# Optimization experiments

Measured on AMD Instinct MI355X. Metric: run time of the kernel, lower is better.

## Reference

```python
import jax, jax.numpy as jnp
import numpy as np

S, N, F, H, D, E, EL = 3, 100000, 64, 64, 64, 1000000, 500000
DP = 0.4


def setup_inputs() -> dict:
    key = jax.random.key(0)
    ks = jax.random.split(key, 12)
    inp = {
        'x': jax.random.normal(ks[0], (S, N, F), dtype=jnp.float32),
        'edge_index': jax.random.randint(ks[1], (S, 2, E), 0, N, dtype=jnp.int64 if jax.config.jax_enable_x64 else jnp.int32),
        'layer_edge_index': jax.random.randint(ks[2], (S - 1, 2, EL), 0, N, dtype=jnp.int64 if jax.config.jax_enable_x64 else jnp.int32),
        'deg_scalar': jax.random.uniform(ks[3], (S - 1,), minval=1.0, maxval=16.0, dtype=jnp.float32),
        'layer_W1': jax.random.normal(ks[4], (S, F, H), dtype=jnp.float32) * 0.05,
        'layer_b1': jnp.zeros((S, H), dtype=jnp.float32),
        'layer_W2': jax.random.normal(ks[5], (S, H, D), dtype=jnp.float32) * 0.05,
        'layer_b2': jnp.zeros((S, D), dtype=jnp.float32),
        'pred_W1': jax.random.normal(ks[6], (D, H), dtype=jnp.float32) * 0.05,
        'pred_b1': jnp.zeros((H,), dtype=jnp.float32),
        'pred_W2': jax.random.normal(ks[7], (H, 2), dtype=jnp.float32) * 0.05,
        'pred_b2': jnp.zeros((2,), dtype=jnp.float32),
    }
    return inp


def gcn_conv(h_in, src, dst, W, b, n):
    # standard GCNConv: D^-1/2 (A+I) D^-1/2 (X W) + b, messages flow src->dst
    h = h_in @ W  # [n, d_out]
    loop = jnp.arange(n, dtype=src.dtype)
    src2 = jnp.concatenate([src, loop])
    dst2 = jnp.concatenate([dst, loop])
    deg = jax.ops.segment_sum(jnp.ones_like(dst2, dtype=h.dtype), dst2, num_segments=n)
    dinv = jax.lax.rsqrt(jnp.maximum(deg, 1.0))  # self-loops guarantee deg>=1
    coef = (dinv[src2] * dinv[dst2])[:, None]
    out = jax.ops.segment_sum(h[src2] * coef, dst2, num_segments=n)
    return out + b


def gcn_net(x, ei, W1, b1, W2, b2, n):
    h = jax.nn.relu(gcn_conv(x, ei[0], ei[1], W1, b1, n))
    return gcn_conv(h, ei[0], ei[1], W2, b2, n)


def reference(x, edge_index, layer_edge_index, deg_scalar,
              layer_W1, layer_b1, layer_W2, layer_b2,
              pred_W1, pred_b1, pred_W2, pred_b2):
    last = None
    for i in range(S):
        lf = gcn_net(x[i], edge_index[i], layer_W1[i], layer_b1[i], layer_W2[i], layer_b2[i], N)  # [N, D]
        if i == 0:
            last = lf  # first surface: degrees empty -> no cross-layer aggregation
        else:
            recv, src = layer_edge_index[i - 1][0], layer_edge_index[i - 1][1]
            agg = lf + jax.ops.segment_sum(last[src], recv, num_segments=N)
            last = agg / deg_scalar[i - 1]  # faithful to source: scalar degrees[i]
    # F.dropout with default training=True -> active dropout; fixed key for determinism
    keep = jax.random.bernoulli(jax.random.key(42), 1.0 - DP, last.shape)
    x_emb = jnp.where(keep, last / (1.0 - DP), 0.0).astype(last.dtype)
    return gcn_net(x_emb, edge_index[-1], pred_W1, pred_b1, pred_W2, pred_b2, N)  # [N, 2]
```

## Files before the change

kernel.cpp:

```cpp
#include <hip/hip_runtime.h>
#include <hip/hip_fp16.h>

#define NN 100000
#define EE 1000000
#define ELL 500000
#define NF (NN*64)
#define NB_SCAN ((NN + 1023) / 1024)

#define OFF_CNT    100352
#define OFF_BSUM   200704
#define OFF_RPA    200832
#define OFF_COLA   301184
#define OFF_RPB    1301184
#define OFF_COLB   1401536
#define WS_SINGLE  (1301184 + 3*NF)
#define WS_DUAL    (2401536 + 4*NF)

__device__ __forceinline__ void threefry2x32(unsigned k0, unsigned k1, unsigned &x0, unsigned &x1){
  unsigned ks2 = k0 ^ k1 ^ 0x1BD11BDAu;
#define TF_R(R) { x0 += x1; x1 = (x1<<(R))|(x1>>(32-(R))); x1 ^= x0; }
  x0 += k0; x1 += k1;
  TF_R(13) TF_R(15) TF_R(26) TF_R(6)
  x0 += k1;  x1 += ks2 + 1u;
  TF_R(17) TF_R(29) TF_R(16) TF_R(24)
  x0 += ks2; x1 += k0 + 2u;
  TF_R(13) TF_R(15) TF_R(26) TF_R(6)
  x0 += k0;  x1 += k1 + 3u;
  TF_R(17) TF_R(29) TF_R(16) TF_R(24)
  x0 += k1;  x1 += ks2 + 4u;
  TF_R(13) TF_R(15) TF_R(26) TF_R(6)
  x0 += ks2; x1 += k0 + 5u;
#undef TF_R
}

__device__ __forceinline__ float dropout_val(float v, unsigned i){
  unsigned x0 = 0u, x1 = i;
  threefry2x32(0u, 42u, x0, x1);
  unsigned bits = x0 ^ x1;
  float u = __uint_as_float((bits >> 9) | 0x3f800000u) - 1.0f;
  return (u < 0.6f) ? v * (1.0f/0.6f) : 0.0f;
}

__global__ void k_probe(const int* __restrict__ ei, unsigned hostbits, float* __restrict__ out){
  if (threadIdx.x != 0 || blockIdx.x != 0) return;
  unsigned bits = hostbits;
  { unsigned a=0u, b=0u; threefry2x32(0u, 0u, a, b);
    if (a != 0x6b200159u || b != 0x99ba4efeu) bits |= 1u; }
  if (bits) out[0] = 1.0e4f * (float)bits;
}

__device__ __forceinline__ uint2 f4_to_h4(float4 v){
  __half2 lo = __floats2half2_rn(v.x, v.y);
  __half2 hi = __floats2half2_rn(v.z, v.w);
  uint2 r; r.x = *(unsigned*)&lo; r.y = *(unsigned*)&hi; return r;
}
__device__ __forceinline__ float4 h4_to_f4(uint2 u){
  __half2 lo = *(__half2*)&u.x;
  __half2 hi = *(__half2*)&u.y;
  float2 a = __half22float2(lo), b = __half22float2(hi);
  return make_float4(a.x, a.y, b.x, b.y);
}

__global__ void k_zero_int(int* __restrict__ p, int n){
  int i = blockIdx.x*256 + threadIdx.x;
  if (i < n) p[i] = 0;
}

__global__ void k_zerof(int* __restrict__ cnt, int n, int* __restrict__ flag){
  int i = blockIdx.x*256 + threadIdx.x;
  if (i < n) cnt[i] = 0;
  if (i == 0) *flag = 0;
}

__global__ void k_deg(const int* __restrict__ dst, int ne, int* __restrict__ cnt){
  int i = blockIdx.x*256 + threadIdx.x;
  if (i < ne) atomicAdd(&cnt[dst[i]], 1);
}

__global__ void k_degrank(const int* __restrict__ dst, int ne, int* __restrict__ cnt,
                          int* __restrict__ rank){
  int i = blockIdx.x*256 + threadIdx.x;
  if (i >= ne) return;
  rank[i] = atomicAdd(&cnt[dst[i]], 1);
}

__global__ void k_dinv(const int* __restrict__ cnt, float* __restrict__ dinv, int n){
  int i = blockIdx.x*256 + threadIdx.x;
  if (i < n) dinv[i] = 1.0f / sqrtf((float)(cnt[i] + 1));
}

__global__ __launch_bounds__(1024) void k_scanfused(const int* __restrict__ cnt, int* __restrict__ bsum,
                                                    int* __restrict__ flag, int* __restrict__ rowptr,
                                                    float* __restrict__ dinv, int computeDinv, int n){
  __shared__ int lds[1024];
  __shared__ int ps[128];
  int t = threadIdx.x;
  int i = blockIdx.x*1024 + t;
  int v = (i < n) ? cnt[i] : 0;
  if (computeDinv && i < n) dinv[i] = 1.0f / sqrtf((float)(v + 1));
  lds[t] = v;
  __syncthreads();
  for (int off = 1; off < 1024; off <<= 1){
    int x = (t >= off) ? lds[t - off] : 0;
    __syncthreads();
    lds[t] += x;
    __syncthreads();
  }
  int incl = lds[t];
  if (t == 1023){
    bsum[blockIdx.x] = lds[1023];
    __threadfence();
    atomicAdd(flag, 1);
  }
  if (t == 0){
    while (atomicAdd(flag, 0) < NB_SCAN) { }
  }
  __syncthreads();
  if (t < 128) ps[t] = (t < blockIdx.x) ? bsum[t] : 0;
  __syncthreads();
  if (t < 64) ps[t] += ps[t + 64];
  __syncthreads();
  if (t < 32) ps[t] += ps[t + 32];
  __syncthreads();
  if (t < 16) ps[t] += ps[t + 16];
  __syncthreads();
  if (t < 8)  ps[t] += ps[t + 8];
  __syncthreads();
  if (t < 4)  ps[t] += ps[t + 4];
  __syncthreads();
  if (t < 2)  ps[t] += ps[t + 2];
  __syncthreads();
  if (t < 1)  ps[t] += ps[t + 1];
  __syncthreads();
  int excl = incl - v + ps[0];
  if (i < n)  rowptr[i] = excl;
  if (i == n-1) rowptr[n] = excl + v;
}

__global__ void k_fillrz(const int* __restrict__ src, const int* __restrict__ dst, int ne,
                         const int* __restrict__ rowptr, const int* __restrict__ rank,
                         int* __restrict__ col, int* __restrict__ cnt, int* __restrict__ flag){
  int e = blockIdx.x*256 + threadIdx.x;
  if (e < NN) cnt[e] = 0;
  if (e == 0) *flag = 0;
  if (e >= ne) return;
  col[rowptr[dst[e]] + rank[e]] = src[e];
}

__global__ void k_fillr(const int* __restrict__ src, const int* __restrict__ dst, int ne,
                        const int* __restrict__ rowptr, const int* __restrict__ rank,
                        int* __restrict__ col){
  int e = blockIdx.x*256 + threadIdx.x;
  if (e >= ne) return;
  col[rowptr[dst[e]] + rank[e]] = src[e];
}

template<bool RELU, bool SCALE>
__global__ __launch_bounds__(256) void k_gemm64(const float* __restrict__ X, const float* __restrict__ W,
                                                const float* __restrict__ dinv,
                                                int nrows, float* __restrict__ Y){
  __shared__ float Ws[64][64];
  int t = threadIdx.x;
  {
    const float4* W4 = (const float4*)W;
    float4* S4 = (float4*)&Ws[0][0];
    #pragma unroll
    for (int i = 0; i < 4; ++i) S4[t + 256*i] = W4[t + 256*i];
  }
  __syncthreads();
  int row = blockIdx.x*16 + (t>>4);
  if (row >= nrows) return;
  int c0 = (t & 15) * 4;
  const float4* Xr = (const float4*)(X + (size_t)row*64);
  float4 acc = make_float4(0.f,0.f,0.f,0.f);
  #pragma unroll
  for (int kk = 0; kk < 16; ++kk){
    float4 xv = Xr[kk];
    if (RELU){
      xv.x = fmaxf(xv.x, 0.f); xv.y = fmaxf(xv.y, 0.f);
      xv.z = fmaxf(xv.z, 0.f); xv.w = fmaxf(xv.w, 0.f);
    }
    int k = kk*4;
    float4 w0 = *(const float4*)&Ws[k+0][c0];
    float4 w1 = *(const float4*)&Ws[k+1][c0];
    float4 w2 = *(const float4*)&Ws[k+2][c0];
    float4 w3 = *(const float4*)&Ws[k+3][c0];
    acc.x = fmaf(xv.x, w0.x, acc.x); acc.y = fmaf(xv.x, w0.y, acc.y);
    acc.z = fmaf(xv.x, w0.z, acc.z); acc.w = fmaf(xv.x, w0.w, acc.w);
    acc.x = fmaf(xv.y, w1.x, acc.x); acc.y = fmaf(xv.y, w1.y, acc.y);
    acc.z = fmaf(xv.y, w1.z, acc.z); acc.w = fmaf(xv.y, w1.w, acc.w);
    acc.x = fmaf(xv.z, w2.x, acc.x); acc.y = fmaf(xv.z, w2.y, acc.y);
    acc.z = fmaf(xv.z, w2.z, acc.z); acc.w = fmaf(xv.z, w2.w, acc.w);
    acc.x = fmaf(xv.w, w3.x, acc.x); acc.y = fmaf(xv.w, w3.y, acc.y);
    acc.z = fmaf(xv.w, w3.z, acc.z); acc.w = fmaf(xv.w, w3.w, acc.w);
  }
  if (SCALE){
    float dv = dinv[row];
    acc.x *= dv; acc.y *= dv; acc.z *= dv; acc.w *= dv;
  }
  *(float4*)(Y + (size_t)row*64 + c0) = acc;
}

template<bool RELU>
__global__ __launch_bounds__(256) void k_gemm64h(const float* __restrict__ X, const float* __restrict__ W,
                                                 const float* __restrict__ dinv,
                                                 int nrows, uint2* __restrict__ Y16){
  __shared__ float Ws[64][64];
  int t = threadIdx.x;
  {
    const float4* W4 = (const float4*)W;
    float4* S4 = (float4*)&Ws[0][0];
    #pragma unroll
    for (int i = 0; i < 4; ++i) S4[t + 256*i] = W4[t + 256*i];
  }
  __syncthreads();
  int row = blockIdx.x*16 + (t>>4);
  if (row >= nrows) return;
  int c0 = (t & 15) * 4;
  const float4* Xr = (const float4*)(X + (size_t)row*64);
  float4 acc = make_float4(0.f,0.f,0.f,0.f);
  #pragma unroll
  for (int kk = 0; kk < 16; ++kk){
    float4 xv = Xr[kk];
    if (RELU){
      xv.x = fmaxf(xv.x, 0.f); xv.y = fmaxf(xv.y, 0.f);
      xv.z = fmaxf(xv.z, 0.f); xv.w = fmaxf(xv.w, 0.f);
    }
    int k = kk*4;
    float4 w0 = *(const float4*)&Ws[k+0][c0];
    float4 w1 = *(const float4*)&Ws[k+1][c0];
    float4 w2 = *(const float4*)&Ws[k+2][c0];
    float4 w3 = *(const float4*)&Ws[k+3][c0];
    acc.x = fmaf(xv.x, w0.x, acc.x); acc.y = fmaf(xv.x, w0.y, acc.y);
    acc.z = fmaf(xv.x, w0.z, acc.z); acc.w = fmaf(xv.x, w0.w, acc.w);
    acc.x = fmaf(xv.y, w1.x, acc.x); acc.y = fmaf(xv.y, w1.y, acc.y);
    acc.z = fmaf(xv.y, w1.z, acc.z); acc.w = fmaf(xv.y, w1.w, acc.w);
    acc.x = fmaf(xv.z, w2.x, acc.x); acc.y = fmaf(xv.z, w2.y, acc.y);
    acc.z = fmaf(xv.z, w2.z, acc.z); acc.w = fmaf(xv.z, w2.w, acc.w);
    acc.x = fmaf(xv.w, w3.x, acc.x); acc.y = fmaf(xv.w, w3.y, acc.y);
    acc.z = fmaf(xv.w, w3.z, acc.z); acc.w = fmaf(xv.w, w3.w, acc.w);
  }
  float dv = dinv[row];
  acc.x *= dv; acc.y *= dv; acc.z *= dv; acc.w *= dv;
  Y16[(size_t)row*16 + (t & 15)] = f4_to_h4(acc);
}

template<bool RELU, bool SCALE>
__global__ __launch_bounds__(256) void k_gemm2(const float* __restrict__ X, const float* __restrict__ W,
                                               const float* __restrict__ dinv,
                                               int nrows, float* __restrict__ Y){
  __shared__ float Ws[128];
  int t = threadIdx.x;
  if (t < 128) Ws[t] = W[t];
  __syncthreads();
  int row = blockIdx.x*256 + t;
  if (row >= nrows) return;
  const float4* Xr = (const float4*)(X + (size_t)row*64);
  float a0 = 0.f, a1 = 0.f;
  #pragma unroll
  for (int kk = 0; kk < 16; ++kk){
    float4 xv = Xr[kk];
    if (RELU){ xv.x=fmaxf(xv.x,0.f); xv.y=fmaxf(xv.y,0.f); xv.z=fmaxf(xv.z,0.f); xv.w=fmaxf(xv.w,0.f); }
    int k = kk*4;
    a0 = fmaf(xv.x, Ws[2*k+0], a0); a1 = fmaf(xv.x, Ws[2*k+1], a1);
    a0 = fmaf(xv.y, Ws[2*k+2], a0); a1 = fmaf(xv.y, Ws[2*k+3], a1);
    a0 = fmaf(xv.z, Ws[2*k+4], a0); a1 = fmaf(xv.z, Ws[2*k+5], a1);
    a0 = fmaf(xv.w, Ws[2*k+6], a0); a1 = fmaf(xv.w, Ws[2*k+7], a1);
  }
  if (SCALE){ float dv = dinv[row]; a0 *= dv; a1 *= dv; }
  Y[(size_t)row*2]   = a0;
  Y[(size_t)row*2+1] = a1;
}

__device__ __forceinline__ float4 gather_rows4(const int* __restrict__ col, int beg, int end,
                                               const float4* __restrict__ h4, int fq, float4 acc){
  int j = beg;
  bool p0 = j   < end; int c0 = p0 ? col[j]   : 0;
  bool p1 = j+1 < end; int c1 = p1 ? col[j+1] : 0;
  bool p2 = j+2 < end; int c2 = p2 ? col[j+2] : 0;
  bool p3 = j+3 < end; int c3 = p3 ? col[j+3] : 0;
  while (p0){
    float4 v0 = h4[(size_t)c0*16 + fq];
    float4 v1 = p1 ? h4[(size_t)c1*16 + fq] : make_float4(0.f,0.f,0.f,0.f);
    float4 v2 = p2 ? h4[(size_t)c2*16 + fq] : make_float4(0.f,0.f,0.f,0.f);
    float4 v3 = p3 ? h4[(size_t)c3*16 + fq] : make_float4(0.f,0.f,0.f,0.f);
    j += 4;
    bool q0 = j < end, q1 = j+1 < end, q2 = j+2 < end, q3 = j+3 < end;
    int n0 = q0 ? col[j]   : 0;
    int n1 = q1 ? col[j+1] : 0;
    int n2 = q2 ? col[j+2] : 0;
    int n3 = q3 ? col[j+3] : 0;
    acc.x += v0.x + v1.x + v2.x + v3.x;
    acc.y += v0.y + v1.y + v2.y + v3.y;
    acc.z += v0.z + v1.z + v2.z + v3.z;
    acc.w += v0.w + v1.w + v2.w + v3.w;
    p0=q0; p1=q1; p2=q2; p3=q3; c0=n0; c1=n1; c2=n2; c3=n3;
  }
  return acc;
}

__device__ __forceinline__ float4 gather_rows4_h16(const int* __restrict__ col, int beg, int end,
                                                   const uint2* __restrict__ h16, int fq, float4 acc){
  int j = beg;
  bool p0 = j   < end; int c0 = p0 ? col[j]   : 0;
  bool p1 = j+1 < end; int c1 = p1 ? col[j+1] : 0;
  bool p2 = j+2 < end; int c2 = p2 ? col[j+2] : 0;
  bool p3 = j+3 < end; int c3 = p3 ? col[j+3] : 0;
  const uint2 z = make_uint2(0u, 0u);
  while (p0){
    uint2 u0 = h16[(size_t)c0*16 + fq];
    uint2 u1 = p1 ? h16[(size_t)c1*16 + fq] : z;
    uint2 u2 = p2 ? h16[(size_t)c2*16 + fq] : z;
    uint2 u3 = p3 ? h16[(size_t)c3*16 + fq] : z;
    j += 4;
    bool q0 = j < end, q1 = j+1 < end, q2 = j+2 < end, q3 = j+3 < end;
    int n0 = q0 ? col[j]   : 0;
    int n1 = q1 ? col[j+1] : 0;
    int n2 = q2 ? col[j+2] : 0;
    int n3 = q3 ? col[j+3] : 0;
    float4 v0 = h4_to_f4(u0), v1 = h4_to_f4(u1), v2 = h4_to_f4(u2), v3 = h4_to_f4(u3);
    acc.x += v0.x + v1.x + v2.x + v3.x;
    acc.y += v0.y + v1.y + v2.y + v3.y;
    acc.z += v0.z + v1.z + v2.z + v3.z;
    acc.w += v0.w + v1.w + v2.w + v3.w;
    p0=q0; p1=q1; p2=q2; p3=q3; c0=n0; c1=n1; c2=n2; c3=n3;
  }
  return acc;
}

__global__ __launch_bounds__(256) void k_gather64(const int* __restrict__ rowptr, const int* __restrict__ col,
                                                  const float* __restrict__ h, const float* __restrict__ dinv,
                                                  const float* __restrict__ b, float* __restrict__ out){
  int gt = blockIdx.x*256 + threadIdx.x;
  int fq = gt & 15;
  int node = gt >> 4;
  if (node >= NN) return;
  const float4* __restrict__ h4 = (const float4*)h;
  float4 acc = h4[(size_t)node*16 + fq];
  acc = gather_rows4(col, rowptr[node], rowptr[node+1], h4, fq, acc);
  float dv = dinv[node];
  float4 bb = ((const float4*)b)[fq];
  float4 r;
  r.x = fmaf(acc.x, dv, bb.x); r.y = fmaf(acc.y, dv, bb.y);
  r.z = fmaf(acc.z, dv, bb.z); r.w = fmaf(acc.w, dv, bb.w);
  *(float4*)(out + (size_t)node*64 + fq*4) = r;
}

__global__ __launch_bounds__(256) void k_gather64h(const int* __restrict__ rowptr, const int* __restrict__ col,
                                                   const uint2* __restrict__ h16, const float* __restrict__ dinv,
                                                   const float* __restrict__ b, float* __restrict__ out){
  int gt = blockIdx.x*256 + threadIdx.x;
  int fq = gt & 15;
  int node = gt >> 4;
  if (node >= NN) return;
  float4 acc = h4_to_f4(h16[(size_t)node*16 + fq]);
  acc = gather_rows4_h16(col, rowptr[node], rowptr[node+1], h16, fq, acc);
  float dv = dinv[node];
  float4 bb = ((const float4*)b)[fq];
  float4 r;
  r.x = fmaf(acc.x, dv, bb.x); r.y = fmaf(acc.y, dv, bb.y);
  r.z = fmaf(acc.z, dv, bb.z); r.w = fmaf(acc.w, dv, bb.w);
  *(float4*)(out + (size_t)node*64 + fq*4) = r;
}

__global__ __launch_bounds__(256) void k_gathergemmh(const int* __restrict__ rowptr, const int* __restrict__ col,
                                                     const uint2* __restrict__ h16, const float* __restrict__ dinv,
                                                     const float* __restrict__ b1, const float* __restrict__ W2,
                                                     uint2* __restrict__ Y16){
  __shared__ float Ws[64][64];
  __shared__ float rows[16][68];
  int t = threadIdx.x;
  {
    const float4* W4 = (const float4*)W2;
    float4* S4 = (float4*)&Ws[0][0];
    #pragma unroll
    for (int i = 0; i < 4; ++i) S4[t + 256*i] = W4[t + 256*i];
  }
  __syncthreads();
  int fq = t & 15, grp = t >> 4;
  int node = blockIdx.x*16 + grp;
  bool alive = node < NN;
  float dv = 0.f;
  if (alive){
    float4 acc = h4_to_f4(h16[(size_t)node*16 + fq]);
    acc = gather_rows4_h16(col, rowptr[node], rowptr[node+1], h16, fq, acc);
    dv = dinv[node];
    float4 bb = ((const float4*)b1)[fq];
    float4 r;
    r.x = fmaxf(fmaf(acc.x, dv, bb.x), 0.f);
    r.y = fmaxf(fmaf(acc.y, dv, bb.y), 0.f);
    r.z = fmaxf(fmaf(acc.z, dv, bb.z), 0.f);
    r.w = fmaxf(fmaf(acc.w, dv, bb.w), 0.f);
    *(float4*)&rows[grp][fq*4] = r;
  }
  __syncthreads();
  if (alive){
    const float* __restrict__ row = &rows[grp][0];
    float4 o = make_float4(0.f,0.f,0.f,0.f);
    int c0 = fq*4;
    #pragma unroll 8
    for (int k = 0; k < 64; ++k){
      float rv = row[k];
      float4 w = *(const float4*)&Ws[k][c0];
      o.x = fmaf(rv, w.x, o.x); o.y = fmaf(rv, w.y, o.y);
      o.z = fmaf(rv, w.z, o.z); o.w = fmaf(rv, w.w, o.w);
    }
    o.x *= dv; o.y *= dv; o.z *= dv; o.w *= dv;
    Y16[(size_t)node*16 + fq] = f4_to_h4(o);
  }
}

__global__ __launch_bounds__(256) void k_gathergemm(const int* __restrict__ rowptr, const int* __restrict__ col,
                                                    const float* __restrict__ h, const float* __restrict__ dinv,
                                                    const float* __restrict__ b1, const float* __restrict__ W2,
                                                    float* __restrict__ Y){
  __shared__ float Ws[64][64];
  __shared__ float rows[16][68];
  int t = threadIdx.x;
  {
    const float4* W4 = (const float4*)W2;
    float4* S4 = (float4*)&Ws[0][0];
    #pragma unroll
    for (int i = 0; i < 4; ++i) S4[t + 256*i] = W4[t + 256*i];
  }
  __syncthreads();
  int fq = t & 15, grp = t >> 4;
  int node = blockIdx.x*16 + grp;
  bool alive = node < NN;
  float dv = 0.f;
  if (alive){
    const float4* __restrict__ h4 = (const float4*)h;
    float4 acc = h4[(size_t)node*16 + fq];
    acc = gather_rows4(col, rowptr[node], rowptr[node+1], h4, fq, acc);
    dv = dinv[node];
    float4 bb = ((const float4*)b1)[fq];
    float4 r;
    r.x = fmaxf(fmaf(acc.x, dv, bb.x), 0.f);
    r.y = fmaxf(fmaf(acc.y, dv, bb.y), 0.f);
    r.z = fmaxf(fmaf(acc.z, dv, bb.z), 0.f);
    r.w = fmaxf(fmaf(acc.w, dv, bb.w), 0.f);
    *(float4*)&rows[grp][fq*4] = r;
  }
  __syncthreads();
  if (alive){
    const float* __restrict__ row = &rows[grp][0];
    float4 o = make_float4(0.f,0.f,0.f,0.f);
    int c0 = fq*4;
    #pragma unroll 8
    for (int k = 0; k < 64; ++k){
      float rv = row[k];
      float4 w = *(const float4*)&Ws[k][c0];
      o.x = fmaf(rv, w.x, o.x); o.y = fmaf(rv, w.y, o.y);
      o.z = fmaf(rv, w.z, o.z); o.w = fmaf(rv, w.w, o.w);
    }
    o.x *= dv; o.y *= dv; o.z *= dv; o.w *= dv;
    *(float4*)(Y + (size_t)node*64 + fq*4) = o;
  }
}

template<bool DROP>
__global__ __launch_bounds__(256) void k_gatherlfaggh(const int* __restrict__ rpA, const int* __restrict__ colA,
                                                      const uint2* __restrict__ h16, const float* __restrict__ dinv,
                                                      const float* __restrict__ b,
                                                      const int* __restrict__ rpB, const int* __restrict__ colB,
                                                      const float* __restrict__ last,
                                                      const float* __restrict__ ds, int dsidx,
                                                      float* __restrict__ out){
  int gt = blockIdx.x*256 + threadIdx.x;
  int fq = gt & 15;
  int node = gt >> 4;
  if (node >= NN) return;
  float4 acc = h4_to_f4(h16[(size_t)node*16 + fq]);
  acc = gather_rows4_h16(colA, rpA[node], rpA[node+1], h16, fq, acc);
  float dv = dinv[node];
  float4 bb = ((const float4*)b)[fq];
  float4 lf;
  lf.x = fmaf(acc.x, dv, bb.x); lf.y = fmaf(acc.y, dv, bb.y);
  lf.z = fmaf(acc.z, dv, bb.z); lf.w = fmaf(acc.w, dv, bb.w);
  float4 agg = gather_rows4(colB, rpB[node], rpB[node+1], (const float4*)last, fq,
                            make_float4(0.f,0.f,0.f,0.f));
  float inv = 1.0f / ds[dsidx];
  float4 r;
  r.x = (lf.x + agg.x) * inv; r.y = (lf.y + agg.y) * inv;
  r.z = (lf.z + agg.z) * inv; r.w = (lf.w + agg.w) * inv;
  if (DROP){
    unsigned base_i = (unsigned)node*64u + (unsigned)fq*4u;
    r.x = dropout_val(r.x, base_i + 0);
    r.y = dropout_val(r.y, base_i + 1);
    r.z = dropout_val(r.z, base_i + 2);
    r.w = dropout_val(r.w, base_i + 3);
  }
  *(float4*)(out + (size_t)node*64 + fq*4) = r;
}

template<bool DROP>
__global__ __launch_bounds__(256) void k_agggather(const int* __restrict__ rowptr, const int* __restrict__ col,
                                                    const float* __restrict__ lf, const float* __restrict__ last,
                                                    const float* __restrict__ ds, int dsidx, float* __restrict__ out){
  int gt = blockIdx.x*256 + threadIdx.x;
  int fq = gt & 15;
  int node = gt >> 4;
  if (node >= NN) return;
  float4 acc = ((const float4*)lf)[(size_t)node*16 + fq];
  acc = gather_rows4(col, rowptr[node], rowptr[node+1], (const float4*)last, fq, acc);
  float inv = 1.0f / ds[dsidx];
  float4 r;
  r.x = acc.x * inv; r.y = acc.y * inv; r.z = acc.z * inv; r.w = acc.w * inv;
  if (DROP){
    unsigned base_i = (unsigned)node*64u + (unsigned)fq*4u;
    r.x = dropout_val(r.x, base_i + 0);
    r.y = dropout_val(r.y, base_i + 1);
    r.z = dropout_val(r.z, base_i + 2);
    r.w = dropout_val(r.w, base_i + 3);
  }
  *(float4*)(out + (size_t)node*64 + fq*4) = r;
}

__global__ void k_gather2(const int* __restrict__ rowptr, const int* __restrict__ col,
                          const float* __restrict__ h2, const float* __restrict__ dinv,
                          const float* __restrict__ b, float* __restrict__ out){
  int d = blockIdx.x*256 + threadIdx.x;
  if (d >= NN) return;
  int beg = rowptr[d], end = rowptr[d+1];
  float a0 = h2[(size_t)d*2];
  float a1 = h2[(size_t)d*2+1];
  for (int j = beg; j < end; ++j){
    int s = col[j];
    a0 += h2[(size_t)s*2];
    a1 += h2[(size_t)s*2+1];
  }
  float dv = dinv[d];
  out[(size_t)d*2]   = fmaf(a0, dv, b[0]);
  out[(size_t)d*2+1] = fmaf(a1, dv, b[1]);
}

__global__ void k_dropout(const float* __restrict__ last, float* __restrict__ xemb){
  unsigned i = blockIdx.x*256 + threadIdx.x;
  if (i >= NF) return;
  xemb[i] = dropout_val(last[i], i);
}

__global__ void k_convinit(const float* __restrict__ h, const float* __restrict__ dinv,
                           const float* __restrict__ b, float* __restrict__ out){
  int i = blockIdx.x*256 + threadIdx.x;
  if (i >= NF) return;
  int v = i >> 6, c = i & 63;
  float dv = dinv[v];
  out[i] = h[i]*dv*dv + b[c];
}
__global__ void k_scatter64(const int* __restrict__ src, const int* __restrict__ dst, int ne,
                            const float* __restrict__ h, const float* __restrict__ dinv,
                            float* __restrict__ out){
  int lane = threadIdx.x & 63;
  int wid  = (blockIdx.x*256 + threadIdx.x) >> 6;
  int nw   = (gridDim.x*256) >> 6;
  for (int e = wid; e < ne; e += nw){
    int s = src[e], d = dst[e];
    float coef = dinv[s]*dinv[d];
    atomicAdd(&out[d*64 + lane], h[s*64 + lane]*coef);
  }
}
__global__ void k_layeragg(const int* __restrict__ recv, const int* __restrict__ srcn, int ne,
                           const float* __restrict__ last, float* __restrict__ acc){
  int lane = threadIdx.x & 63;
  int wid  = (blockIdx.x*256 + threadIdx.x) >> 6;
  int nw   = (gridDim.x*256) >> 6;
  for (int e = wid; e < ne; e += nw){
    int r = recv[e], s = srcn[e];
    atomicAdd(&acc[r*64 + lane], last[s*64 + lane]);
  }
}
__global__ void k_scale(const float* __restrict__ in, const float* __restrict__ ds, int dsidx,
                        float* __restrict__ out){
  int i = blockIdx.x*256 + threadIdx.x;
  if (i < NF) out[i] = in[i] / ds[dsidx];
}
__global__ void k_convinit2(const float* __restrict__ h2, const float* __restrict__ dinv,
                            const float* __restrict__ b, float* __restrict__ out){
  int i = blockIdx.x*256 + threadIdx.x;
  if (i >= NN*2) return;
  int v = i >> 1, c = i & 1;
  float dv = dinv[v];
  out[i] = h2[i]*dv*dv + b[c];
}
__global__ void k_scatter2(const int* __restrict__ src, const int* __restrict__ dst, int ne,
                           const float* __restrict__ h2, const float* __restrict__ dinv,
                           float* __restrict__ out){
  int e = blockIdx.x*256 + threadIdx.x;
  if (e >= ne) return;
  int s = src[e], d = dst[e];
  float coef = dinv[s]*dinv[d];
  atomicAdd(&out[d*2 + 0], h2[s*2 + 0]*coef);
  atomicAdd(&out[d*2 + 1], h2[s*2 + 1]*coef);
}

extern "C" void kernel_launch(void* const* d_in, const int* in_sizes, int n_in,
                              void* d_out, int out_size, void* d_ws, size_t ws_size,
                              hipStream_t stream) {
  const float* x    = (const float*)d_in[0];
  const int*   ei   = (const int*)  d_in[1];
  const int*   lei  = (const int*)  d_in[2];
  const float* degs = (const float*)d_in[3];
  const float* lW1  = (const float*)d_in[4];
  const float* lb1  = (const float*)d_in[5];
  const float* lW2  = (const float*)d_in[6];
  const float* lb2  = (const float*)d_in[7];
  const float* pW1  = (const float*)d_in[8];
  const float* pb1  = (const float*)d_in[9];
  const float* pW2  = (const float*)d_in[10];
  const float* pb2  = (const float*)d_in[11];
  float* out = (float*)d_out;

  const int gN  = (NN + 255)/256;
  const int gE  = (EE + 255)/256;
  const int gEL = (ELL + 255)/256;
  const int gNF = (NF + 255)/256;
  const int gG16 = (NN*16 + 255)/256;

  const bool dual   = ws_size >= (size_t)WS_DUAL * 4;
  const bool single = ws_size >= (size_t)WS_SINGLE * 4;

  if (dual) {
    float* base   = (float*)d_ws;
    float* dinv   = base;
    int*   cnt    = (int*)(base + OFF_CNT);
    int*   bsum   = (int*)(base + OFF_BSUM);
    int*   flag   = bsum + 120;
    int*   rpA    = (int*)(base + OFF_RPA);
    int*   colA   = (int*)(base + OFF_COLA);
    int*   rpB    = (int*)(base + OFF_RPB);
    int*   colB   = (int*)(base + OFF_COLB);
    float* F0     = base + OFF_COLB + 1000000;
    float* F1     = F0 + NF;
    float* F2     = F1 + NF;
    uint2* H0     = (uint2*)(F2 + NF);
    uint2* H1     = H0 + (size_t)NN*16;

    auto build_csr = [&](const int* srcp, const int* dstp, int ne, int gEdges, int computeDinv,
                         int* rowptr, int* col, int* rank){
      k_degrank<<<gEdges, 256, 0, stream>>>(dstp, ne, cnt, rank);
      k_scanfused<<<NB_SCAN, 1024, 0, stream>>>(cnt, bsum, flag, rowptr, dinv, computeDinv, NN);
      k_fillrz<<<gEdges, 256, 0, stream>>>(srcp, dstp, ne, rowptr, rank, col, cnt, flag);
    };

    const int* s0 = ei;                  const int* d0 = s0 + EE;
    const int* s1 = ei + 2*(size_t)EE;   const int* d1 = s1 + EE;
    const int* s2 = ei + 4*(size_t)EE;   const int* d2 = s2 + EE;
    const int* r0 = lei;                 const int* ls0 = r0 + ELL;
    const int* r1 = lei + 2*(size_t)ELL; const int* ls1 = r1 + ELL;

    k_zerof<<<gN, 256, 0, stream>>>(cnt, NN, flag);

    build_csr(s0, d0, EE, gE, 1, rpA, colA, (int*)F0);
    k_gemm64h<false><<<6250, 256, 0, stream>>>(x, lW1, dinv, NN, H0);
    k_gathergemmh<<<6250, 256, 0, stream>>>(rpA, colA, H0, dinv, lb1, lW2, H1);
    k_gather64h<<<gG16, 256, 0, stream>>>(rpA, colA, H1, dinv, lb2, F2);
    build_csr(s1, d1, EE, gE, 1, rpA, colA, (int*)F0);
    build_csr(ls0, r0, ELL, gEL, 0, rpB, colB, (int*)F0);
    k_gemm64h<false><<<6250, 256, 0, stream>>>(x + (size_t)NF, lW1 + 4096, dinv, NN, H0);
    k_gathergemmh<<<6250, 256, 0, stream>>>(rpA, colA, H0, dinv, lb1 + 64, lW2 + 4096, H1);
    k_gatherlfaggh<false><<<gG16, 256, 0, stream>>>(rpA, colA, H1, dinv, lb2 + 64,
                                                    rpB, colB, F2, degs, 0, F0);
    build_csr(s2, d2, EE, gE, 1, rpA, colA, (int*)F1);
    build_csr(ls1, r1, ELL, gEL, 0, rpB, colB, (int*)F1);
    k_gemm64h<false><<<6250, 256, 0, stream>>>(x + 2*(size_t)NF, lW1 + 8192, dinv, NN, H0);
    k_gathergemmh<<<6250, 256, 0, stream>>>(rpA, colA, H0, dinv, lb1 + 128, lW2 + 8192, H1);
    k_gatherlfaggh<true><<<gG16, 256, 0, stream>>>(rpA, colA, H1, dinv, lb2 + 128,
                                                   rpB, colB, F0, degs, 1, F1);
    k_gemm64h<false><<<6250, 256, 0, stream>>>(F1, pW1, dinv, NN, H0);
    k_gather64h<<<gG16, 256, 0, stream>>>(rpA, colA, H0, dinv, pb1, F2);
    k_gemm2<true,true><<<gN, 256, 0, stream>>>(F2, pW2, dinv, NN, F1);
    k_gather2<<<gN, 256, 0, stream>>>(rpA, colA, F1, dinv, pb2, out);
    k_probe<<<1, 64, 0, stream>>>(ei, 0u, out);
    return;
  }

  if (single) {
    float* base   = (float*)d_ws;
    float* dinv   = base;
    int*   cnt    = (int*)(base + OFF_CNT);
    int*   bsum   = (int*)(base + OFF_BSUM);
    int*   flag   = bsum + 120;
    int*   rpA    = (int*)(base + OFF_RPA);
    int*   colA   = (int*)(base + OFF_COLA);
    float* F0     = base + OFF_RPB;
    float* F1     = F0 + NF;
    float* F2     = F1 + NF;

    auto build_csr = [&](const int* srcp, const int* dstp, int ne, int gEdges, int computeDinv,
                         int* rowptr, int* col, int* rank){
      k_zerof<<<gN, 256, 0, stream>>>(cnt, NN, flag);
      k_degrank<<<gEdges, 256, 0, stream>>>(dstp, ne, cnt, rank);
      k_scanfused<<<NB_SCAN, 1024, 0, stream>>>(cnt, bsum, flag, rowptr, dinv, computeDinv, NN);
      k_fillr<<<gEdges, 256, 0, stream>>>(srcp, dstp, ne, rowptr, rank, col);
    };

    const int* s0 = ei;                  const int* d0 = s0 + EE;
    const int* s1 = ei + 2*(size_t)EE;   const int* d1 = s1 + EE;
    const int* s2 = ei + 4*(size_t)EE;   const int* d2 = s2 + EE;
    const int* r0 = lei;                 const int* ls0 = r0 + ELL;
    const int* r1 = lei + 2*(size_t)ELL; const int* ls1 = r1 + ELL;

    build_csr(s0, d0, EE, gE, 1, rpA, colA, (int*)F0);
    k_gemm64<false,true><<<6250, 256, 0, stream>>>(x, lW1, dinv, NN, F0);
    k_gathergemm<<<6250, 256, 0, stream>>>(rpA, colA, F0, dinv, lb1, lW2, F1);
    k_gather64<<<gG16, 256, 0, stream>>>(rpA, colA, F1, dinv, lb2, F2);
    build_csr(s1, d1, EE, gE, 1, rpA, colA, (int*)F0);
    k_gemm64<false,true><<<6250, 256, 0, stream>>>(x + (size_t)NF, lW1 + 4096, dinv, NN, F0);
    k_gathergemm<<<6250, 256, 0, stream>>>(rpA, colA, F0, dinv, lb1 + 64, lW2 + 4096, F1);
    build_csr(ls0, r0, ELL, gEL, 0, rpA, colA, (int*)F0);
    k_agggather<false><<<gG16, 256, 0, stream>>>(rpA, colA, F1, F2, degs, 0, F0);
    build_csr(s2, d2, EE, gE, 1, rpA, colA, (int*)F1);
    k_gemm64<false,true><<<6250, 256, 0, stream>>>(x + 2*(size_t)NF, lW1 + 8192, dinv, NN, F1);
    k_gathergemm<<<6250, 256, 0, stream>>>(rpA, colA, F1, dinv, lb1 + 128, lW2 + 8192, F2);
    build_csr(ls1, r1, ELL, gEL, 0, rpA, colA, (int*)F1);
    k_agggather<true><<<gG16, 256, 0, stream>>>(rpA, colA, F2, F0, degs, 1, F1);
    build_csr(s2, d2, EE, gE, 0, rpA, colA, (int*)F0);
    k_gemm64<false,true><<<6250, 256, 0, stream>>>(F1, pW1, dinv, NN, F0);
    k_gather64<<<gG16, 256, 0, stream>>>(rpA, colA, F0, dinv, pb1, F2);
    k_gemm2<true,true><<<gN, 256, 0, stream>>>(F2, pW2, dinv, NN, F1);
    k_gather2<<<gN, 256, 0, stream>>>(rpA, colA, F1, dinv, pb2, out);
    k_probe<<<1, 64, 0, stream>>>(ei, 0u, out);
    return;
  }

  float* base = (float*)d_ws;
  float* dinv = base;
  int*   cnt  = (int*)(base + 100352);
  float* A    = base + 262144;
  float* B    = A + NF;
  float* C    = B + NF;

  for (int i = 0; i < 3; ++i){
    const int* srcp = ei + (size_t)i*2*EE;
    const int* dstp = srcp + EE;
    k_zero_int<<<gN, 256, 0, stream>>>(cnt, NN);
    k_deg<<<gE, 256, 0, stream>>>(dstp, EE, cnt);
    k_dinv<<<gN, 256, 0, stream>>>(cnt, dinv, NN);
    k_gemm64<false,false><<<6250, 256, 0, stream>>>(x + (size_t)i*NF, lW1 + (size_t)i*64*64, dinv, NN, A);
    k_convinit<<<gNF, 256, 0, stream>>>(A, dinv, lb1 + (size_t)i*64, B);
    k_scatter64<<<8192, 256, 0, stream>>>(srcp, dstp, EE, A, dinv, B);
    k_gemm64<true,false><<<6250, 256, 0, stream>>>(B, lW2 + (size_t)i*64*64, dinv, NN, A);
    float* T = (i == 0) ? C : B;
    k_convinit<<<gNF, 256, 0, stream>>>(A, dinv, lb2 + (size_t)i*64, T);
    k_scatter64<<<8192, 256, 0, stream>>>(srcp, dstp, EE, A, dinv, T);
    if (i > 0){
      const int* recvp = lei + (size_t)(i-1)*2*ELL;
      const int* lsrcp = recvp + ELL;
      k_layeragg<<<4096, 256, 0, stream>>>(recvp, lsrcp, ELL, C, B);
      k_scale<<<gNF, 256, 0, stream>>>(B, degs, i-1, C);
    }
  }
  k_dropout<<<gNF, 256, 0, stream>>>(C, B);
  const int* srcp = ei + (size_t)2*2*EE;
  const int* dstp = srcp + EE;
  k_gemm64<false,false><<<6250, 256, 0, stream>>>(B, pW1, dinv, NN, A);
  k_convinit<<<gNF, 256, 0, stream>>>(A, dinv, pb1, C);
  k_scatter64<<<8192, 256, 0, stream>>>(srcp, dstp, EE, A, dinv, C);
  k_gemm2<true,false><<<gN, 256, 0, stream>>>(C, pW2, dinv, NN, B);
  k_convinit2<<<(NN*2 + 255)/256, 256, 0, stream>>>(B, dinv, pb2, out);
  k_scatter2<<<gE, 256, 0, stream>>>(srcp, dstp, EE, B, dinv, out);
  k_probe<<<1, 64, 0, stream>>>(ei, 0u, out);
}
```

Before: 645.7 us.

## Store cross-layer features in fp16 and fuse predictor gather with second GEMM

Intermediate per-surface layer features (last) are now written and gathered as half precision instead of fp32, which halves the bytes moved by the cross-layer segment-sum gathers. The predictor's first-layer gather is fused with the ReLU and the 64x2 projection using lane shuffles, removing a full fp32 N x 64 write/read and the separate k_gemm2 launch. Workspace grows by one feature buffer. The cost is reduced numerical precision on intermediate embeddings.

```diff
diff --git a/kernel.cpp b/kernel.cpp
--- a/kernel.cpp
+++ b/kernel.cpp
@@ -14,7 +14,7 @@
 #define OFF_RPB    1301184
 #define OFF_COLB   1401536
 #define WS_SINGLE  (1301184 + 3*NF)
-#define WS_DUAL    (2401536 + 4*NF)
+#define WS_DUAL    (2401536 + 5*NF)
 
 __device__ __forceinline__ void threefry2x32(unsigned k0, unsigned k1, unsigned &x0, unsigned &x1){
   unsigned ks2 = k0 ^ k1 ^ 0x1BD11BDAu;
@@ -346,9 +346,9 @@
   *(float4*)(out + (size_t)node*64 + fq*4) = r;
 }
 
-__global__ __launch_bounds__(256) void k_gather64h(const int* __restrict__ rowptr, const int* __restrict__ col,
-                                                   const uint2* __restrict__ h16, const float* __restrict__ dinv,
-                                                   const float* __restrict__ b, float* __restrict__ out){
+__global__ __launch_bounds__(256) void k_gather64hh(const int* __restrict__ rowptr, const int* __restrict__ col,
+                                                    const uint2* __restrict__ h16, const float* __restrict__ dinv,
+                                                    const float* __restrict__ b, uint2* __restrict__ out16){
   int gt = blockIdx.x*256 + threadIdx.x;
   int fq = gt & 15;
   int node = gt >> 4;
@@ -360,7 +360,7 @@
   float4 r;
   r.x = fmaf(acc.x, dv, bb.x); r.y = fmaf(acc.y, dv, bb.y);
   r.z = fmaf(acc.z, dv, bb.z); r.w = fmaf(acc.w, dv, bb.w);
-  *(float4*)(out + (size_t)node*64 + fq*4) = r;
+  out16[(size_t)node*16 + fq] = f4_to_h4(r);
 }
 
 __global__ __launch_bounds__(256) void k_gathergemmh(const int* __restrict__ rowptr, const int* __restrict__ col,
@@ -458,14 +458,14 @@
   }
 }
 
-template<bool DROP>
-__global__ __launch_bounds__(256) void k_gatherlfaggh(const int* __restrict__ rpA, const int* __restrict__ colA,
-                                                      const uint2* __restrict__ h16, const float* __restrict__ dinv,
-                                                      const float* __restrict__ b,
-                                                      const int* __restrict__ rpB, const int* __restrict__ colB,
-                                                      const float* __restrict__ last,
-                                                      const float* __restrict__ ds, int dsidx,
-                                                      float* __restrict__ out){
+template<bool DROP, bool OUT16>
+__global__ __launch_bounds__(256) void k_gatherlfagg2h(const int* __restrict__ rpA, const int* __restrict__ colA,
+                                                       const uint2* __restrict__ h16, const float* __restrict__ dinv,
+                                                       const float* __restrict__ b,
+                                                       const int* __restrict__ rpB, const int* __restrict__ colB,
+                                                       const uint2* __restrict__ last16,
+                                                       const float* __restrict__ ds, int dsidx,
+                                                       void* __restrict__ outv){
   int gt = blockIdx.x*256 + threadIdx.x;
   int fq = gt & 15;
   int node = gt >> 4;
@@ -477,8 +477,8 @@
   float4 lf;
   lf.x = fmaf(acc.x, dv, bb.x); lf.y = fmaf(acc.y, dv, bb.y);
   lf.z = fmaf(acc.z, dv, bb.z); lf.w = fmaf(acc.w, dv, bb.w);
-  float4 agg = gather_rows4(colB, rpB[node], rpB[node+1], (const float4*)last, fq,
-                            make_float4(0.f,0.f,0.f,0.f));
+  float4 agg = gather_rows4_h16(colB, rpB[node], rpB[node+1], last16, fq,
+                                make_float4(0.f,0.f,0.f,0.f));
   float inv = 1.0f / ds[dsidx];
   float4 r;
   r.x = (lf.x + agg.x) * inv; r.y = (lf.y + agg.y) * inv;
@@ -490,7 +490,8 @@
     r.z = dropout_val(r.z, base_i + 2);
     r.w = dropout_val(r.w, base_i + 3);
   }
-  *(float4*)(out + (size_t)node*64 + fq*4) = r;
+  if (OUT16) ((uint2*)outv)[(size_t)node*16 + fq] = f4_to_h4(r);
+  else       *(float4*)((float*)outv + (size_t)node*64 + fq*4) = r;
 }
 
 template<bool DROP>
@@ -516,6 +517,37 @@
   *(float4*)(out + (size_t)node*64 + fq*4) = r;
 }
 
+__global__ __launch_bounds__(256) void k_predgather2h(const int* __restrict__ rowptr, const int* __restrict__ col,
+                                                      const uint2* __restrict__ h16, const float* __restrict__ dinv,
+                                                      const float* __restrict__ b1, const float* __restrict__ W2,
+                                                      float* __restrict__ Y){
+  int gt = blockIdx.x*256 + threadIdx.x;
+  int fq = gt & 15;
+  int node = gt >> 4;
+  if (node >= NN) return;
+  float4 acc = h4_to_f4(h16[(size_t)node*16 + fq]);
+  acc = gather_rows4_h16(col, rowptr[node], rowptr[node+1], h16, fq, acc);
+  float dv = dinv[node];
+  float4 bb = ((const float4*)b1)[fq];
+  float4 r;
+  r.x = fmaxf(fmaf(acc.x, dv, bb.x), 0.f);
+  r.y = fmaxf(fmaf(acc.y, dv, bb.y), 0.f);
+  r.z = fmaxf(fmaf(acc.z, dv, bb.z), 0.f);
+  r.w = fmaxf(fmaf(acc.w, dv, bb.w), 0.f);
+  const float4* w4 = (const float4*)W2;
+  float4 wa = w4[fq*2], wb = w4[fq*2 + 1];
+  float o0 = r.x*wa.x + r.y*wa.z + r.z*wb.x + r.w*wb.z;
+  float o1 = r.x*wa.y + r.y*wa.w + r.z*wb.y + r.w*wb.w;
+  o0 += __shfl_xor(o0, 1); o1 += __shfl_xor(o1, 1);
+  o0 += __shfl_xor(o0, 2); o1 += __shfl_xor(o1, 2);
+  o0 += __shfl_xor(o0, 4); o1 += __shfl_xor(o1, 4);
+  o0 += __shfl_xor(o0, 8); o1 += __shfl_xor(o1, 8);
+  if (fq == 0){
+    Y[(size_t)node*2]   = o0 * dv;
+    Y[(size_t)node*2+1] = o1 * dv;
+  }
+}
+
 __global__ void k_gather2(const int* __restrict__ rowptr, const int* __restrict__ col,
                           const float* __restrict__ h2, const float* __restrict__ dinv,
                           const float* __restrict__ b, float* __restrict__ out){
@@ -635,6 +667,8 @@
     float* F2     = F1 + NF;
     uint2* H0     = (uint2*)(F2 + NF);
     uint2* H1     = H0 + (size_t)NN*16;
+    uint2* H2     = H1 + (size_t)NN*16;
+    uint2* H3     = H2 + (size_t)NN*16;
 
     auto build_csr = [&](const int* srcp, const int* dstp, int ne, int gEdges, int computeDinv,
                          int* rowptr, int* col, int* rank){
@@ -654,23 +688,22 @@
     build_csr(s0, d0, EE, gE, 1, rpA, colA, (int*)F0);
     k_gemm64h<false><<<6250, 256, 0, stream>>>(x, lW1, dinv, NN, H0);
     k_gathergemmh<<<6250, 256, 0, stream>>>(rpA, colA, H0, dinv, lb1, lW2, H1);
-    k_gather64h<<<gG16, 256, 0, stream>>>(rpA, colA, H1, dinv, lb2, F2);
+    k_gather64hh<<<gG16, 256, 0, stream>>>(rpA, colA, H1, dinv, lb2, H2);
     build_csr(s1, d1, EE, gE, 1, rpA, colA, (int*)F0);
     build_csr(ls0, r0, ELL, gEL, 0, rpB, colB, (int*)F0);
     k_gemm64h<false><<<6250, 256, 0, stream>>>(x + (size_t)NF, lW1 + 4096, dinv, NN, H0);
     k_gathergemmh<<<6250, 256, 0, stream>>>(rpA, colA, H0, dinv, lb1 + 64, lW2 + 4096, H1);
-    k_gatherlfaggh<false><<<gG16, 256, 0, stream>>>(rpA, colA, H1, dinv, lb2 + 64,
-                                                    rpB, colB, F2, degs, 0, F0);
-    build_csr(s2, d2, EE, gE, 1, rpA, colA, (int*)F1);
-    build_csr(ls1, r1, ELL, gEL, 0, rpB, colB, (int*)F1);
+    k_gatherlfagg2h<false,true><<<gG16, 256, 0, stream>>>(rpA, colA, H1, dinv, lb2 + 64,
+                                                          rpB, colB, H2, degs, 0, (void*)H3);
+    build_csr(s2, d2, EE, gE, 1, rpA, colA, (int*)F0);
+    build_csr(ls1, r1, ELL, gEL, 0, rpB, colB, (int*)F0);
     k_gemm64h<false><<<6250, 256, 0, stream>>>(x + 2*(size_t)NF, lW1 + 8192, dinv, NN, H0);
     k_gathergemmh<<<6250, 256, 0, stream>>>(rpA, colA, H0, dinv, lb1 + 128, lW2 + 8192, H1);
-    k_gatherlfaggh<true><<<gG16, 256, 0, stream>>>(rpA, colA, H1, dinv, lb2 + 128,
-                                                   rpB, colB, F0, degs, 1, F1);
+    k_gatherlfagg2h<true,false><<<gG16, 256, 0, stream>>>(rpA, colA, H1, dinv, lb2 + 128,
+                                                          rpB, colB, H3, degs, 1, (void*)F1);
     k_gemm64h<false><<<6250, 256, 0, stream>>>(F1, pW1, dinv, NN, H0);
-    k_gather64h<<<gG16, 256, 0, stream>>>(rpA, colA, H0, dinv, pb1, F2);
-    k_gemm2<true,true><<<gN, 256, 0, stream>>>(F2, pW2, dinv, NN, F1);
-    k_gather2<<<gN, 256, 0, stream>>>(rpA, colA, F1, dinv, pb2, out);
+    k_predgather2h<<<gG16, 256, 0, stream>>>(rpA, colA, H0, dinv, pb1, pW2, F2);
+    k_gather2<<<gN, 256, 0, stream>>>(rpA, colA, F2, dinv, pb2, out);
     k_probe<<<1, 64, 0, stream>>>(ei, 0u, out);
     return;
   }
```

Measured after the change: 630.5 us. 2.4% less time.
